# Optimization experiments

Hardware: AMD Instinct MI355X
Metric: run time of the kernel (lower is better)

## Reference

```python
import jax, jax.numpy as jnp
import numpy as np

B, P, ENC = 64, 196, 2048
H, A, E, V, T = 512, 512, 512, 10000, 20


def setup_inputs() -> dict:
    key = jax.random.key(0)
    ks = jax.random.split(key, 24)
    s = 0.02
    inp = {
        "encoder_out": jax.random.normal(ks[0], (B, P, ENC), jnp.float32),
        "captions": jax.random.randint(ks[1], (B, T), 0, V),
        "lengths": jnp.sort(jax.random.randint(ks[2], (B,), 5, T + 1))[::-1].at[0].set(T).astype(jnp.int32),
        # Attention
        "enc_att_w": jax.random.normal(ks[3], (A, ENC)) * s,
        "enc_att_b": jnp.zeros((A,)),
        "hid_att_w": jax.random.normal(ks[4], (A, H)) * s,
        "hid_att_b": jnp.zeros((A,)),
        "full_att_w": jax.random.normal(ks[5], (1, A)) * s,
        "full_att_b": jnp.zeros((1,)),
        # Embedding
        "embed_w": jax.random.uniform(ks[6], (V, E), minval=-0.1, maxval=0.1),
        # LSTMCell (input = embed + encoder -> E + ENC)
        "lstm_w_ih": jax.random.normal(ks[7], (4 * H, E + ENC)) * s,
        "lstm_w_hh": jax.random.normal(ks[8], (4 * H, H)) * s,
        "lstm_b_ih": jnp.zeros((4 * H,)),
        "lstm_b_hh": jnp.zeros((4 * H,)),
        # init hidden/cell from mean encoder features
        "init_h_w": jax.random.normal(ks[9], (H, ENC)) * s,
        "init_h_b": jnp.zeros((H,)),
        "init_c_w": jax.random.normal(ks[10], (H, ENC)) * s,
        "init_c_b": jnp.zeros((H,)),
        # gating
        "fbeta_w": jax.random.normal(ks[11], (ENC, H)) * s,
        "fbeta_b": jnp.zeros((ENC,)),
        # output fc
        "fc_w": jax.random.uniform(ks[12], (V, H), minval=-0.1, maxval=0.1),
        "fc_b": jnp.zeros((V,)),
    }
    return inp


def reference(encoder_out, captions, lengths,
              enc_att_w, enc_att_b, hid_att_w, hid_att_b, full_att_w, full_att_b,
              embed_w, lstm_w_ih, lstm_w_hh, lstm_b_ih, lstm_b_hh,
              init_h_w, init_h_b, init_c_w, init_c_b,
              fbeta_w, fbeta_b, fc_w, fc_b):
    emb = embed_w[captions]                      # [B, T, E]
    mean_enc = encoder_out.mean(axis=1)          # [B, ENC]
    h0 = mean_enc @ init_h_w.T + init_h_b
    c0 = mean_enc @ init_c_w.T + init_c_b
    # encoder attention projection is constant across timesteps
    att1 = encoder_out @ enc_att_w.T + enc_att_b  # [B, P, A]
    dec_len = lengths - 1                         # decode lengths per sample

    def step(carry, xs):
        h, c = carry
        emb_t, t = xs
        att2 = h @ hid_att_w.T + hid_att_b                     # [B, A]
        e = jax.nn.relu(att1 + att2[:, None, :]) @ full_att_w[0] + full_att_b[0]  # [B, P]
        alpha = jax.nn.softmax(e, axis=1)                       # [B, P]
        awe = jnp.einsum('bpe,bp->be', encoder_out, alpha)      # [B, ENC]
        gate = jax.nn.sigmoid(h @ fbeta_w.T + fbeta_b)
        x = jnp.concatenate([emb_t, gate * awe], axis=1)        # [B, E+ENC]
        gates = x @ lstm_w_ih.T + lstm_b_ih + h @ lstm_w_hh.T + lstm_b_hh
        i, f, g, o = jnp.split(gates, 4, axis=1)
        c_new = jax.nn.sigmoid(f) * c + jax.nn.sigmoid(i) * jnp.tanh(g)
        h_new = jax.nn.sigmoid(o) * jnp.tanh(c_new)
        pred = h_new @ fc_w.T + fc_b                            # [B, V]
        active = (t < dec_len)[:, None]
        h = jnp.where(active, h_new, h)
        c = jnp.where(active, c_new, c)
        pred = jnp.where(active, pred, jnp.zeros_like(pred))
        alpha = jnp.where(active, alpha, jnp.zeros_like(alpha))
        return (h, c), (pred, alpha)

    Tm1 = emb.shape[1] - 1
    ts = jnp.arange(Tm1)
    emb_seq = jnp.transpose(emb[:, :Tm1], (1, 0, 2))            # [T-1, B, E]
    (_, _), (preds, alphas) = jax.lax.scan(step, (h0, c0), (emb_seq, ts))
    predictions = jnp.transpose(preds, (1, 0, 2))               # [B, T-1, V]
    alphas = jnp.transpose(alphas, (1, 0, 2))                   # [B, T-1, P]
    return predictions, alphas
```

## Files before the change

kernel.cpp:

```cpp
#include <hip/hip_runtime.h>
#include <hip/hip_bf16.h>

typedef short short8  __attribute__((ext_vector_type(8)));
typedef float floatx4 __attribute__((ext_vector_type(4)));
typedef int   int4v   __attribute__((ext_vector_type(4)));

constexpr int BB = 64, PP = 196, CENC = 2048, HH = 512, AA = 512, EE = 512;
constexpr int VV = 10000, TT = 20, TM1 = 19;
constexpr int NCAT = 4608;

__device__ __forceinline__ float bf2f(short u) {
    union { unsigned u; float f; } v; v.u = ((unsigned)(unsigned short)u) << 16; return v.f;
}
__device__ __forceinline__ short f2bf(float f) {
    union { float f; unsigned u; } v; v.f = f;
    unsigned r = v.u + 0x7FFF + ((v.u >> 16) & 1);
    return (short)(r >> 16);
}

#define GLL(gp, lp) __builtin_amdgcn_global_load_lds( \
    (const __attribute__((address_space(1))) void*)(gp), \
    (__attribute__((address_space(3))) void*)(lp), 16, 0, 0)

__global__ __launch_bounds__(256)
void kPrepW(const float* __restrict__ encw_s, const float* __restrict__ haw,
            const float* __restrict__ fbw, const float* __restrict__ whh,
            const float* __restrict__ wih, const float* __restrict__ fcw,
            const float* __restrict__ ihw, const float* __restrict__ icw,
            const float* __restrict__ hab, const float* __restrict__ fbb,
            const float* __restrict__ bih, const float* __restrict__ bhh,
            const float* __restrict__ ihb, const float* __restrict__ icb,
            short* __restrict__ encw_d, short* __restrict__ wcat_d,
            short* __restrict__ wihe_d, short* __restrict__ wihm_d,
            short* __restrict__ fc_d, short* __restrict__ initW_d,
            float* __restrict__ biascat, float* __restrict__ biasg,
            float* __restrict__ biasInit)
{
    long e = ((long)blockIdx.x * 256 + threadIdx.x) * 8;
    const float* sp = nullptr; short* dp = nullptr; long de = 0;
    if (e < 1048576)       { sp = &encw_s[e]; dp = encw_d; de = e; }
    else if (e < 3407872)  { long u = e - 1048576; long row = u >> 9, col = u & 511;
                             sp = (row < 512) ? &haw[row * 512 + col]
                                : (row < 2560) ? &fbw[(row - 512) * 512 + col]
                                               : &whh[(row - 2560) * 512 + col];
                             dp = wcat_d; de = u; }
    else if (e < 7602176)  { long u = e - 3407872; long row = u >> 11, col = u & 2047;
                             sp = &wih[row * 2560 + 512 + col]; dp = wihe_d; de = u; }
    else if (e < 8650752)  { long u = e - 7602176; long row = u >> 9, col = u & 511;
                             sp = &wih[row * 2560 + col]; dp = wihm_d; de = u; }
    else if (e < 13770752) { long u = e - 8650752; sp = &fcw[u]; dp = fc_d; de = u; }
    else if (e < 15867904) { long u = e - 13770752;
                             sp = (u < 1048576) ? &ihw[u] : &icw[u - 1048576];
                             dp = initW_d; de = u; }
    else if (e < 15872512) { long u = e - 15867904;
                             for (int j = 0; j < 8; ++j) { long w = u + j;
                                 biascat[w] = (w < 512) ? hab[w] : ((w < 2560) ? fbb[w - 512] : 0.f); }
                             return; }
    else if (e < 15874560) { long u = e - 15872512;
                             for (int j = 0; j < 8; ++j) biasg[u + j] = bih[u + j] + bhh[u + j];
                             return; }
    else if (e < 15875584) { long u = e - 15874560;
                             for (int j = 0; j < 8; ++j) { long w = u + j;
                                 biasInit[w] = (w < 512) ? ihb[w] : icb[w - 512]; }
                             return; }
    else return;
    union { short s[8]; int4v v; } u8;
    #pragma unroll
    for (int j = 0; j < 8; ++j) u8.s[j] = f2bf(sp[j]);
    *reinterpret_cast<int4v*>(&dp[de]) = u8.v;
}

template<int FULL>
__global__ __launch_bounds__(256)
void kMeanEnc(const float* __restrict__ enc, short* __restrict__ enc16,
              float* __restrict__ meanP)
{
    int b = blockIdx.x, kc = blockIdx.y, pz = blockIdx.z;
    int k = kc * 256 + threadIdx.x;
    const float* eb = &enc[((size_t)b * PP + pz * 28) * CENC + k];
    short* ob = &enc16[((size_t)b * PP + pz * 28) * CENC + k];
    float s0 = 0, s1 = 0, s2 = 0, s3 = 0;
    for (int p = 0; p < 28; p += 4) {
        float v0 = eb[(size_t)(p + 0) * CENC], v1 = eb[(size_t)(p + 1) * CENC];
        float v2 = eb[(size_t)(p + 2) * CENC], v3 = eb[(size_t)(p + 3) * CENC];
        s0 += v0; s1 += v1; s2 += v2; s3 += v3;
        if (FULL) {
            ob[(size_t)(p + 0) * CENC] = f2bf(v0); ob[(size_t)(p + 1) * CENC] = f2bf(v1);
            ob[(size_t)(p + 2) * CENC] = f2bf(v2); ob[(size_t)(p + 3) * CENC] = f2bf(v3);
        }
    }
    meanP[((size_t)pz * 64 + b) * 2048 + k] = (s0 + s1) + (s2 + s3);
}

__global__ __launch_bounds__(256)
void kReduceMean(const float* __restrict__ meanP, short* __restrict__ mean16)
{
    int b = blockIdx.x, c0 = threadIdx.x * 8;
    const float inv = 1.0f / PP;
    union { short s[8]; int4v v; } u8;
    #pragma unroll
    for (int j = 0; j < 8; ++j) {
        float s = 0.f;
        #pragma unroll
        for (int pz = 0; pz < 7; ++pz) s += meanP[((size_t)pz * 64 + b) * 2048 + c0 + j];
        u8.s[j] = f2bf(s * inv);
    }
    *reinterpret_cast<int4v*>(&mean16[b * 2048 + c0]) = u8.v;
}

__global__ __launch_bounds__(256)
void kEmbGather(const float* __restrict__ embw, const int* __restrict__ captions,
                short* __restrict__ embA)
{
    long e = ((long)blockIdx.x * 256 + threadIdx.x) * 8;
    int r = (int)(e >> 9), j = (int)(e & 511);
    int t = r >> 6, b = r & 63;
    int tok = captions[b * TT + t];
    const float* sp = &embw[(size_t)tok * EE + j];
    union { short s[8]; int4v v; } u8;
    #pragma unroll
    for (int q = 0; q < 8; ++q) u8.s[q] = f2bf(sp[q]);
    *reinterpret_cast<int4v*>(&embA[e]) = u8.v;
}

template<int AOP, int WOP, int EOP, int SWZ>
__global__ __launch_bounds__(256)
void kGemm(const void* __restrict__ Ap, int lda, const short* __restrict__ W, int ldw,
           const float* __restrict__ bias, int Ntot,
           float* __restrict__ outF, int ldc, short* __restrict__ outB,
           int nk, const int* __restrict__ lengths)
{
    __shared__ short As[64 * 64];
    __shared__ short Ws[64 * 64];
    int nb, mb, kz;
    if (SWZ == 0) { nb = blockIdx.x; mb = blockIdx.y; kz = blockIdx.z; }
    else if (SWZ == 1) {
        int j = blockIdx.x;
        if (j < 1536) { mb = (j >> 6) * 8 + (j & 7); nb = (j >> 3) & 7; }
        else          { int u = j - 1536; mb = 192 + (u >> 3); nb = u & 7; }
        kz = 0;
    } else {
        int j = blockIdx.x; int c = j & 7, s = j >> 3;
        mb = s % 19; int u = s / 19; nb = 8 * u + c; kz = 0;
        if (nb * 64 >= Ntot) return;
    }
    const int tid = threadIdx.x;
    const int m0 = mb * 64, n0 = nb * 64, k0 = kz * nk * 64;
    const int w = tid >> 6, l = tid & 63;
    floatx4 acc[4] = {};

    for (int ks = 0; ks < nk; ++ks) {
        int kt = k0 + ks * 64;
        if (AOP == 0) {
            const short* A = (const short*)Ap;
            #pragma unroll
            for (int i = 0; i < 2; ++i) {
                int ii = w * 2 + i;
                int row = ii * 8 + (l >> 3);
                int cg = l & 7;
                const short* gp = &A[(size_t)(m0 + row) * lda + kt + ((cg ^ (row & 7)) << 3)];
                GLL(gp, &As[ii * 512]);
            }
        } else {
            const float* A = (const float*)Ap;
            #pragma unroll
            for (int i = 0; i < 2; ++i) {
                int s = tid + i * 256, row = s >> 3, cg = s & 7;
                const float* sp = &A[(size_t)(m0 + row) * lda + kt + cg * 8];
                float4 a = *reinterpret_cast<const float4*>(sp);
                float4 b = *reinterpret_cast<const float4*>(sp + 4);
                union { short s[8]; int4v v; } u8;
                u8.s[0]=f2bf(a.x); u8.s[1]=f2bf(a.y); u8.s[2]=f2bf(a.z); u8.s[3]=f2bf(a.w);
                u8.s[4]=f2bf(b.x); u8.s[5]=f2bf(b.y); u8.s[6]=f2bf(b.z); u8.s[7]=f2bf(b.w);
                *reinterpret_cast<int4v*>(&As[row * 64 + ((cg ^ (row & 7)) << 3)]) = u8.v;
            }
        }
        #pragma unroll
        for (int i = 0; i < 2; ++i) {
            int ii = w * 2 + i;
            int r = ii * 8 + (l >> 3);
            int cg = l & 7;
            int wr;
            if (WOP == 1) wr = 512 * (r >> 4) + 16 * nb + (r & 15);
            else          wr = n0 + r;
            if (WOP == 1 || wr < Ntot) {
                const short* gp = &W[(size_t)wr * ldw + kt + ((cg ^ (r & 7)) << 3)];
                GLL(gp, &Ws[ii * 512]);
            }
        }
        __syncthreads();
        #pragma unroll
        for (int kc = 0; kc < 2; ++kc) {
            int arow = 16 * w + (l & 15);
            int cg = 4 * kc + (l >> 4);
            short8 af = *reinterpret_cast<const short8*>(&As[arow * 64 + ((cg ^ (arow & 7)) << 3)]);
            #pragma unroll
            for (int q = 0; q < 4; ++q) {
                int wrow = 16 * q + (l & 15);
                short8 wf = *reinterpret_cast<const short8*>(&Ws[wrow * 64 + ((cg ^ (wrow & 7)) << 3)]);
                acc[q] = __builtin_amdgcn_mfma_f32_16x16x32_bf16(af, wf, acc[q], 0, 0, 0);
            }
        }
        __syncthreads();
    }
    int l4 = l >> 4, l15 = l & 15;
    #pragma unroll
    for (int q = 0; q < 4; ++q) {
        #pragma unroll
        for (int j = 0; j < 4; ++j) {
            int m = m0 + 16 * w + 4 * l4 + j;
            int n = n0 + 16 * q + l15;
            float val = acc[q][j];
            if (EOP == 0) {
                outF[(size_t)m * ldc + n] = val + bias[n];
            } else if (EOP == 1) {
                outB[(size_t)m * ldc + n] = f2bf(val + bias[n]);
            } else if (EOP == 2) {
                if (n < Ntot) {
                    int b = m & 63, tt = m >> 6;
                    bool act = tt < (lengths[b] - 1);
                    outF[((size_t)b * TM1 + tt) * VV + n] = act ? (val + bias[n]) : 0.f;
                }
            } else if (EOP == 3) {
                int mloc = m - m0;
                outF[((size_t)kz * 64 + mloc) * ldc + n] = val;
            } else {
                int col = 512 * q + (n0 >> 2) + l15;
                int mloc = m - m0;
                outF[((size_t)kz * 64 + mloc) * 2048 + col] = val;
            }
        }
    }
}

__global__ __launch_bounds__(256)
void kReduceHC(const float* __restrict__ Pc, const float* __restrict__ biasInit,
               float* __restrict__ hc, short* __restrict__ h16)
{
    int b = blockIdx.x, tid = threadIdx.x;
    for (int j = tid; j < 1024; j += 256) {
        float s = Pc[((size_t)0 * BB + b) * 1024 + j] + Pc[((size_t)1 * BB + b) * 1024 + j]
                + Pc[((size_t)2 * BB + b) * 1024 + j] + Pc[((size_t)3 * BB + b) * 1024 + j];
        s += biasInit[j];
        hc[b * 1024 + j] = s;
        if (j < 512) h16[b * 512 + j] = f2bf(s);
    }
}

template<int FULL>
__global__ __launch_bounds__(256)
void kStepBC(const short* __restrict__ att1, const float* __restrict__ P3h,
             const float* __restrict__ faw, const float* __restrict__ fab,
             const int* __restrict__ lengths, const void* __restrict__ encp,
             short* __restrict__ x16, float* __restrict__ alpha_out, int t)
{
    int blk = blockIdx.x, tid = threadIdx.x;
    int b = blk & 63, kc = blk >> 6;
    __shared__ float att2s[512];
    __shared__ float fw[512];
    __shared__ float es[PP];
    __shared__ float alps[PP];
    __shared__ float red[8];
    __shared__ float part[8][256];

    for (int a = tid; a < 512; a += 256) { att2s[a] = P3h[b * NCAT + a]; fw[a] = faw[a]; }
    __syncthreads();

    int wv = tid >> 6, lane = tid & 63;
    for (int p = wv; p < PP; p += 4) {
        short8 v = *reinterpret_cast<const short8*>(&att1[((size_t)b * PP + p) * 512 + lane * 8]);
        float s = 0.f;
        #pragma unroll
        for (int j = 0; j < 8; ++j) {
            float x = bf2f(v[j]) + att2s[lane * 8 + j];
            s += fmaxf(x, 0.f) * fw[lane * 8 + j];
        }
        #pragma unroll
        for (int off = 32; off > 0; off >>= 1) s += __shfl_down(s, off, 64);
        if (lane == 0) es[p] = s + fab[0];
    }
    __syncthreads();
    float m = -1e30f;
    for (int p = tid; p < PP; p += 256) m = fmaxf(m, es[p]);
    #pragma unroll
    for (int off = 32; off > 0; off >>= 1) m = fmaxf(m, __shfl_down(m, off, 64));
    if (lane == 0) red[wv] = m;
    __syncthreads();
    m = fmaxf(fmaxf(red[0], red[1]), fmaxf(red[2], red[3]));
    float ssum = 0.f;
    for (int p = tid; p < PP; p += 256) { float ev = __expf(es[p] - m); es[p] = ev; ssum += ev; }
    #pragma unroll
    for (int off = 32; off > 0; off >>= 1) ssum += __shfl_down(ssum, off, 64);
    if (lane == 0) red[4 + wv] = ssum;
    __syncthreads();
    float inv = 1.f / (red[4] + red[5] + red[6] + red[7]);
    bool active = t < (lengths[b] - 1);
    for (int p = tid; p < PP; p += 256) {
        float al = es[p] * inv;
        alps[p] = al;
        if (kc == 0)
            alpha_out[((size_t)b * TM1 + t) * PP + p] = active ? al : 0.f;
    }
    __syncthreads();

    if (FULL) {
        const short* enc16 = (const short*)encp;
        int g = tid & 31, prow = tid >> 5;
        int k0 = kc * 256 + g * 8;
        float acc[8] = {};
        for (int p = prow; p < PP; p += 8) {
            short8 v = *reinterpret_cast<const short8*>(&enc16[((size_t)b * PP + p) * CENC + k0]);
            float a_ = alps[p];
            #pragma unroll
            for (int j = 0; j < 8; ++j) acc[j] = fmaf(bf2f(v[j]), a_, acc[j]);
        }
        *reinterpret_cast<float4*>(&part[prow][g * 8])     = make_float4(acc[0], acc[1], acc[2], acc[3]);
        *reinterpret_cast<float4*>(&part[prow][g * 8 + 4]) = make_float4(acc[4], acc[5], acc[6], acc[7]);
        __syncthreads();
        int c = tid;
        float awe = 0.f;
        #pragma unroll
        for (int pr = 0; pr < 8; ++pr) awe += part[pr][c];
        int k = kc * 256 + c;
        float gate = 1.f / (1.f + __expf(-P3h[b * NCAT + 512 + k]));
        x16[(size_t)b * CENC + k] = f2bf(gate * awe);
    } else {
        const float* enc = (const float*)encp;
        int g = tid & 63, prow = tid >> 6;
        int k0 = kc * 256 + g * 4;
        float acc[4] = {};
        for (int p = prow; p < PP; p += 4) {
            float4 v = *reinterpret_cast<const float4*>(&enc[((size_t)b * PP + p) * CENC + k0]);
            float a_ = alps[p];
            acc[0] = fmaf(v.x, a_, acc[0]); acc[1] = fmaf(v.y, a_, acc[1]);
            acc[2] = fmaf(v.z, a_, acc[2]); acc[3] = fmaf(v.w, a_, acc[3]);
        }
        *reinterpret_cast<float4*>(&part[prow][g * 4]) = make_float4(acc[0], acc[1], acc[2], acc[3]);
        __syncthreads();
        int c = tid;
        float awe = part[0][c] + part[1][c] + part[2][c] + part[3][c];
        int k = kc * 256 + c;
        float gate = 1.f / (1.f + __expf(-P3h[b * NCAT + 512 + k]));
        x16[(size_t)b * CENC + k] = f2bf(gate * awe);
    }
}

__global__ __launch_bounds__(256)
void kStepD2(const float* __restrict__ Pg, const float* __restrict__ gates_emb,
             const float* __restrict__ P3h, float* __restrict__ hc,
             short* __restrict__ h16, short* __restrict__ allH, int t)
{
    int b = blockIdx.x, tid = threadIdx.x;
    for (int d = tid; d < 512; d += 256) {
        float g4[4];
        #pragma unroll
        for (int q = 0; q < 4; ++q) {
            int col = q * 512 + d;
            float s = gates_emb[((size_t)t * 64 + b) * 2048 + col] + P3h[b * NCAT + 2560 + col];
            #pragma unroll
            for (int kz = 0; kz < 4; ++kz) s += Pg[((size_t)kz * 64 + b) * 2048 + col];
            g4[q] = s;
        }
        float i_ = 1.f / (1.f + __expf(-g4[0]));
        float f_ = 1.f / (1.f + __expf(-g4[1]));
        float g_ = tanhf(g4[2]);
        float o_ = 1.f / (1.f + __expf(-g4[3]));
        float c_new = f_ * hc[b * 1024 + 512 + d] + i_ * g_;
        float h_new = o_ * tanhf(c_new);
        hc[b * 1024 + 512 + d] = c_new;
        hc[b * 1024 + d] = h_new;
        short hb = f2bf(h_new);
        h16[b * 512 + d] = hb;
        allH[((size_t)t * 64 + b) * 512 + d] = hb;
    }
}

extern "C" void kernel_launch(void* const* d_in, const int* in_sizes, int n_in,
                              void* d_out, int out_size, void* d_ws, size_t ws_size,
                              hipStream_t stream)
{
    const float* enc        = (const float*)d_in[0];
    const int*   captions   = (const int*)d_in[1];
    const int*   lengths    = (const int*)d_in[2];
    const float* enc_att_w  = (const float*)d_in[3];
    const float* enc_att_b  = (const float*)d_in[4];
    const float* hid_att_w  = (const float*)d_in[5];
    const float* hid_att_b  = (const float*)d_in[6];
    const float* full_att_w = (const float*)d_in[7];
    const float* full_att_b = (const float*)d_in[8];
    const float* embw       = (const float*)d_in[9];
    const float* w_ih       = (const float*)d_in[10];
    const float* w_hh       = (const float*)d_in[11];
    const float* b_ih       = (const float*)d_in[12];
    const float* b_hh       = (const float*)d_in[13];
    const float* init_h_w   = (const float*)d_in[14];
    const float* init_h_b   = (const float*)d_in[15];
    const float* init_c_w   = (const float*)d_in[16];
    const float* init_c_b   = (const float*)d_in[17];
    const float* fbeta_w    = (const float*)d_in[18];
    const float* fbeta_b    = (const float*)d_in[19];
    const float* fc_w       = (const float*)d_in[20];
    const float* fc_b       = (const float*)d_in[21];

    float* out_pred  = (float*)d_out;
    float* out_alpha = out_pred + (size_t)BB * TM1 * VV;

    char* pr = (char*)d_out;
    short* att1_16   = (short*)pr;  pr += 12845056;
    float* gates_emb = (float*)pr;  pr += 9961472;
    short* wcat16    = (short*)pr;  pr += 4718592;
    short* wihe16    = (short*)pr;  pr += 8388608;
    float* biascat   = (float*)pr;  pr += 18432;
    float* P3h       = (float*)pr;  pr += 1179648;
    float* Pg        = (float*)pr;  pr += 2097152;
    short* embA      = (short*)pr;  pr += 1245184;
    short* wihm16    = (short*)pr;  pr += 2097152;
    short* encw16    = (short*)pr;  pr += 2097152;
    float* biasg     = (float*)pr;  pr += 8192;
    float* meanP     = (float*)pr;  pr += 3670016;
    short* mean16    = (short*)pr;  pr += 262144;

    short* initW16  = (short*)gates_emb;
    float* biasInit = (float*)((char*)gates_emb + 4194304);
    float* hcP      = P3h;

    char* wp = (char*)d_ws;
    float* hc    = (float*)wp;  wp += 262144;
    short* h16   = (short*)wp;  wp += 65536;
    short* x16   = (short*)wp;  wp += 262144;
    short* fc16  = (short*)wp;  wp += 10240000;
    short* allH  = (short*)wp;  wp += 1245184;
    short* enc16 = (short*)wp;  wp += 51380224;
    const bool full = ((size_t)(wp - (char*)d_ws) <= ws_size);

    kPrepW<<<7752, 256, 0, stream>>>(enc_att_w, hid_att_w, fbeta_w, w_hh, w_ih, fc_w,
                                     init_h_w, init_c_w,
                                     hid_att_b, fbeta_b, b_ih, b_hh, init_h_b, init_c_b,
                                     encw16, wcat16, wihe16, wihm16, fc16, initW16,
                                     biascat, biasg, biasInit);
    if (full) kMeanEnc<1><<<dim3(64, 8, 7), 256, 0, stream>>>(enc, enc16, meanP);
    else      kMeanEnc<0><<<dim3(64, 8, 7), 256, 0, stream>>>(enc, enc16, meanP);
    kEmbGather<<<304, 256, 0, stream>>>(embw, captions, embA);
    kReduceMean<<<64, 256, 0, stream>>>(meanP, mean16);

    kGemm<0, 0, 3, 0><<<dim3(16, 1, 4), 256, 0, stream>>>(mean16, CENC, initW16, CENC,
        nullptr, 1024, hcP, 1024, nullptr, 8, nullptr);
    kReduceHC<<<64, 256, 0, stream>>>(hcP, biasInit, hc, h16);

    if (full)
        kGemm<0, 0, 1, 1><<<1568, 256, 0, stream>>>(enc16, CENC, encw16, CENC,
            enc_att_b, 512, nullptr, 512, att1_16, 32, nullptr);
    else
        kGemm<1, 0, 1, 1><<<1568, 256, 0, stream>>>(enc, CENC, encw16, CENC,
            enc_att_b, 512, nullptr, 512, att1_16, 32, nullptr);

    kGemm<0, 0, 0, 0><<<dim3(32, 19, 1), 256, 0, stream>>>(embA, 512, wihm16, 512,
        biasg, 2048, gates_emb, 2048, nullptr, 8, nullptr);

    for (int t = 0; t < TM1; ++t) {
        kGemm<0, 0, 0, 0><<<dim3(72, 1, 1), 256, 0, stream>>>(h16, 512, wcat16, 512,
            biascat, NCAT, P3h, NCAT, nullptr, 8, nullptr);

        if (full) kStepBC<1><<<512, 256, 0, stream>>>(att1_16, P3h, full_att_w,
            full_att_b, lengths, enc16, x16, out_alpha, t);
        else      kStepBC<0><<<512, 256, 0, stream>>>(att1_16, P3h, full_att_w,
            full_att_b, lengths, enc, x16, out_alpha, t);

        kGemm<0, 1, 4, 0><<<dim3(32, 1, 4), 256, 0, stream>>>(x16, CENC, wihe16, CENC,
            nullptr, 2048, Pg, 2048, nullptr, 8, nullptr);

        kStepD2<<<64, 256, 0, stream>>>(Pg, gates_emb, P3h, hc, h16, allH, t);
    }

    kGemm<0, 0, 2, 2><<<3040, 256, 0, stream>>>(allH, 512, fc16, 512,
        fc_b, VV, out_pred, VV, nullptr, 8, lengths);
}
```

Measured before the change: 1.228 ms.

## Restructure decoder step kernels and switch big GEMMs to 128x128 tiles

```diff
diff --git a/kernel.cpp b/kernel.cpp
--- a/kernel.cpp
+++ b/kernel.cpp
@@ -7,7 +7,6 @@
 
 constexpr int BB = 64, PP = 196, CENC = 2048, HH = 512, AA = 512, EE = 512;
 constexpr int VV = 10000, TT = 20, TM1 = 19;
-constexpr int NCAT = 4608;
 
 __device__ __forceinline__ float bf2f(short u) {
     union { unsigned u; float f; } v; v.u = ((unsigned)(unsigned short)u) << 16; return v.f;
@@ -27,44 +26,48 @@
             const float* __restrict__ fbw, const float* __restrict__ whh,
             const float* __restrict__ wih, const float* __restrict__ fcw,
             const float* __restrict__ ihw, const float* __restrict__ icw,
-            const float* __restrict__ hab, const float* __restrict__ fbb,
-            const float* __restrict__ bih, const float* __restrict__ bhh,
-            const float* __restrict__ ihb, const float* __restrict__ icb,
+            const float* __restrict__ fbb, const float* __restrict__ bih,
+            const float* __restrict__ bhh, const float* __restrict__ ihb,
+            const float* __restrict__ icb,
             short* __restrict__ encw_d, short* __restrict__ wcat_d,
             short* __restrict__ wihe_d, short* __restrict__ wihm_d,
             short* __restrict__ fc_d, short* __restrict__ initW_d,
-            float* __restrict__ biascat, float* __restrict__ biasg,
-            float* __restrict__ biasInit)
+            short* __restrict__ hidattT, float* __restrict__ biascat,
+            float* __restrict__ biasg, float* __restrict__ biasInit)
 {
     long e = ((long)blockIdx.x * 256 + threadIdx.x) * 8;
+    union { short s[8]; int4v v; } u8;
     const float* sp = nullptr; short* dp = nullptr; long de = 0;
     if (e < 1048576)       { sp = &encw_s[e]; dp = encw_d; de = e; }
-    else if (e < 3407872)  { long u = e - 1048576; long row = u >> 9, col = u & 511;
-                             sp = (row < 512) ? &haw[row * 512 + col]
-                                : (row < 2560) ? &fbw[(row - 512) * 512 + col]
-                                               : &whh[(row - 2560) * 512 + col];
+    else if (e < 3145728)  { long u = e - 1048576; long row = u >> 9, col = u & 511;
+                             sp = (row < 2048) ? &fbw[row * 512 + col]
+                                               : &whh[(row - 2048) * 512 + col];
                              dp = wcat_d; de = u; }
-    else if (e < 7602176)  { long u = e - 3407872; long row = u >> 11, col = u & 2047;
+    else if (e < 7340032)  { long u = e - 3145728; long row = u >> 11, col = u & 2047;
                              sp = &wih[row * 2560 + 512 + col]; dp = wihe_d; de = u; }
-    else if (e < 8650752)  { long u = e - 7602176; long row = u >> 9, col = u & 511;
+    else if (e < 8388608)  { long u = e - 7340032; long row = u >> 9, col = u & 511;
                              sp = &wih[row * 2560 + col]; dp = wihm_d; de = u; }
-    else if (e < 13770752) { long u = e - 8650752; sp = &fcw[u]; dp = fc_d; de = u; }
-    else if (e < 15867904) { long u = e - 13770752;
+    else if (e < 13508608) { long u = e - 8388608; sp = &fcw[u]; dp = fc_d; de = u; }
+    else if (e < 15605760) { long u = e - 13508608;
                              sp = (u < 1048576) ? &ihw[u] : &icw[u - 1048576];
                              dp = initW_d; de = u; }
-    else if (e < 15872512) { long u = e - 15867904;
+    else if (e < 15867904) { long u = e - 15605760; long k = u >> 9, a0 = u & 511;
+                             #pragma unroll
+                             for (int j = 0; j < 8; ++j) u8.s[j] = f2bf(haw[(a0 + j) * 512 + k]);
+                             *reinterpret_cast<int4v*>(&hidattT[u]) = u8.v;
+                             return; }
+    else if (e < 15872000) { long u = e - 15867904;
                              for (int j = 0; j < 8; ++j) { long w = u + j;
-                                 biascat[w] = (w < 512) ? hab[w] : ((w < 2560) ? fbb[w - 512] : 0.f); }
+                                 biascat[w] = (w < 2048) ? fbb[w] : 0.f; }
                              return; }
-    else if (e < 15874560) { long u = e - 15872512;
+    else if (e < 15874048) { long u = e - 15872000;
                              for (int j = 0; j < 8; ++j) biasg[u + j] = bih[u + j] + bhh[u + j];
                              return; }
-    else if (e < 15875584) { long u = e - 15874560;
+    else if (e < 15875072) { long u = e - 15874048;
                              for (int j = 0; j < 8; ++j) { long w = u + j;
                                  biasInit[w] = (w < 512) ? ihb[w] : icb[w - 512]; }
                              return; }
     else return;
-    union { short s[8]; int4v v; } u8;
     #pragma unroll
     for (int j = 0; j < 8; ++j) u8.s[j] = f2bf(sp[j]);
     *reinterpret_cast<int4v*>(&dp[de]) = u8.v;
@@ -123,27 +126,15 @@
     *reinterpret_cast<int4v*>(&embA[e]) = u8.v;
 }
 
-template<int AOP, int WOP, int EOP, int SWZ>
-__global__ __launch_bounds__(256)
-void kGemm(const void* __restrict__ Ap, int lda, const short* __restrict__ W, int ldw,
-           const float* __restrict__ bias, int Ntot,
-           float* __restrict__ outF, int ldc, short* __restrict__ outB,
-           int nk, const int* __restrict__ lengths)
+template<int EOP>
+__global__ __launch_bounds__(256)
+void kGemm(const short* __restrict__ A, int lda, const short* __restrict__ W, int ldw,
+           const float* __restrict__ bias,
+           float* __restrict__ outF, int ldc, int nk)
 {
     __shared__ short As[64 * 64];
     __shared__ short Ws[64 * 64];
-    int nb, mb, kz;
-    if (SWZ == 0) { nb = blockIdx.x; mb = blockIdx.y; kz = blockIdx.z; }
-    else if (SWZ == 1) {
-        int j = blockIdx.x;
-        if (j < 1536) { mb = (j >> 6) * 8 + (j & 7); nb = (j >> 3) & 7; }
-        else          { int u = j - 1536; mb = 192 + (u >> 3); nb = u & 7; }
-        kz = 0;
-    } else {
-        int j = blockIdx.x; int c = j & 7, s = j >> 3;
-        mb = s % 19; int u = s / 19; nb = 8 * u + c; kz = 0;
-        if (nb * 64 >= Ntot) return;
-    }
+    const int nb = blockIdx.x, mb = blockIdx.y, kz = blockIdx.z;
     const int tid = threadIdx.x;
     const int m0 = mb * 64, n0 = nb * 64, k0 = kz * nk * 64;
     const int w = tid >> 6, l = tid & 63;
@@ -151,20 +142,91 @@
 
     for (int ks = 0; ks < nk; ++ks) {
         int kt = k0 + ks * 64;
+        #pragma unroll
+        for (int i = 0; i < 2; ++i) {
+            int ii = w * 2 + i;
+            int row = ii * 8 + (l >> 3), cg = l & 7;
+            GLL(&A[(size_t)(m0 + row) * lda + kt + ((cg ^ (row & 7)) << 3)], &As[ii * 512]);
+        }
+        #pragma unroll
+        for (int i = 0; i < 2; ++i) {
+            int ii = w * 2 + i;
+            int r = ii * 8 + (l >> 3), cg = l & 7;
+            GLL(&W[(size_t)(n0 + r) * ldw + kt + ((cg ^ (r & 7)) << 3)], &Ws[ii * 512]);
+        }
+        __syncthreads();
+        #pragma unroll
+        for (int kc = 0; kc < 2; ++kc) {
+            int arow = 16 * w + (l & 15);
+            int cg = 4 * kc + (l >> 4);
+            short8 af = *reinterpret_cast<const short8*>(&As[arow * 64 + ((cg ^ (arow & 7)) << 3)]);
+            #pragma unroll
+            for (int q = 0; q < 4; ++q) {
+                int wrow = 16 * q + (l & 15);
+                short8 wf = *reinterpret_cast<const short8*>(&Ws[wrow * 64 + ((cg ^ (wrow & 7)) << 3)]);
+                acc[q] = __builtin_amdgcn_mfma_f32_16x16x32_bf16(af, wf, acc[q], 0, 0, 0);
+            }
+        }
+        __syncthreads();
+    }
+    int l4 = l >> 4, l15 = l & 15;
+    #pragma unroll
+    for (int q = 0; q < 4; ++q) {
+        #pragma unroll
+        for (int j = 0; j < 4; ++j) {
+            int m = m0 + 16 * w + 4 * l4 + j;
+            int n = n0 + 16 * q + l15;
+            float val = acc[q][j];
+            if (EOP == 0) {
+                outF[(size_t)m * ldc + n] = val + bias[n];
+            } else {
+                int mloc = m - m0;
+                outF[((size_t)kz * 64 + mloc) * ldc + n] = val;
+            }
+        }
+    }
+}
+
+template<int AOP, int EOP, int SWZ>
+__global__ __launch_bounds__(256)
+void kGemm128(const void* __restrict__ Ap, int lda, const short* __restrict__ W, int ldw,
+              const float* __restrict__ bias, int Ntot, int Mtot,
+              float* __restrict__ outF, short* __restrict__ outB, int ldc,
+              int nk, const int* __restrict__ lengths)
+{
+    __shared__ short As[128 * 64];
+    __shared__ short Ws[128 * 64];
+    int mb, nb;
+    if (SWZ == 1) {
+        int o = blockIdx.x;
+        int wg = (o & 7) * 49 + (o >> 3);
+        mb = wg >> 2; nb = wg & 3;
+    } else {
+        int o = blockIdx.x;
+        int x = o & 7, idx = o >> 3;
+        int base = (x < 6) ? x * 99 : 594 + (x - 6) * 98;
+        int wg = base + idx;
+        mb = wg % 10; nb = wg / 10;
+    }
+    const int tid = threadIdx.x, w = tid >> 6, l = tid & 63;
+    const int m0 = mb * 128, n0 = nb * 128;
+    const int l4 = l >> 4, l15 = l & 15;
+    floatx4 acc[2][8] = {};
+
+    for (int ks = 0; ks < nk; ++ks) {
+        int kt = ks * 64;
         if (AOP == 0) {
             const short* A = (const short*)Ap;
             #pragma unroll
-            for (int i = 0; i < 2; ++i) {
-                int ii = w * 2 + i;
-                int row = ii * 8 + (l >> 3);
-                int cg = l & 7;
-                const short* gp = &A[(size_t)(m0 + row) * lda + kt + ((cg ^ (row & 7)) << 3)];
-                GLL(gp, &As[ii * 512]);
+            for (int i = 0; i < 4; ++i) {
+                int ii = w * 4 + i;
+                int row = ii * 8 + (l >> 3), cg = l & 7;
+                GLL(&A[(size_t)(m0 + row) * lda + kt + ((cg ^ (row & 7)) << 3)], &As[ii * 512]);
             }
         } else {
             const float* A = (const float*)Ap;
             #pragma unroll
-            for (int i = 0; i < 2; ++i) {
+            for (int i = 0; i < 4; ++i) {
                 int s = tid + i * 256, row = s >> 3, cg = s & 7;
                 const float* sp = &A[(size_t)(m0 + row) * lda + kt + cg * 8];
                 float4 a = *reinterpret_cast<const float4*>(sp);
@@ -176,58 +238,50 @@
             }
         }
         #pragma unroll
-        for (int i = 0; i < 2; ++i) {
-            int ii = w * 2 + i;
-            int r = ii * 8 + (l >> 3);
-            int cg = l & 7;
-            int wr;
-            if (WOP == 1) wr = 512 * (r >> 4) + 16 * nb + (r & 15);
-            else          wr = n0 + r;
-            if (WOP == 1 || wr < Ntot) {
-                const short* gp = &W[(size_t)wr * ldw + kt + ((cg ^ (r & 7)) << 3)];
-                GLL(gp, &Ws[ii * 512]);
-            }
+        for (int i = 0; i < 4; ++i) {
+            int ii = w * 4 + i;
+            int r = ii * 8 + (l >> 3), cg = l & 7;
+            GLL(&W[(size_t)(n0 + r) * ldw + kt + ((cg ^ (r & 7)) << 3)], &Ws[ii * 512]);
         }
         __syncthreads();
         #pragma unroll
         for (int kc = 0; kc < 2; ++kc) {
-            int arow = 16 * w + (l & 15);
-            int cg = 4 * kc + (l >> 4);
-            short8 af = *reinterpret_cast<const short8*>(&As[arow * 64 + ((cg ^ (arow & 7)) << 3)]);
-            #pragma unroll
-            for (int q = 0; q < 4; ++q) {
-                int wrow = 16 * q + (l & 15);
+            int cg = 4 * kc + l4;
+            short8 af0, af1;
+            {
+                int ar0 = 32 * w + l15;
+                int ar1 = 32 * w + 16 + l15;
+                af0 = *reinterpret_cast<const short8*>(&As[ar0 * 64 + ((cg ^ (ar0 & 7)) << 3)]);
+                af1 = *reinterpret_cast<const short8*>(&As[ar1 * 64 + ((cg ^ (ar1 & 7)) << 3)]);
+            }
+            #pragma unroll
+            for (int q = 0; q < 8; ++q) {
+                int wrow = 16 * q + l15;
                 short8 wf = *reinterpret_cast<const short8*>(&Ws[wrow * 64 + ((cg ^ (wrow & 7)) << 3)]);
-                acc[q] = __builtin_amdgcn_mfma_f32_16x16x32_bf16(af, wf, acc[q], 0, 0, 0);
-            }
-        }
-        __syncthreads();
-    }
-    int l4 = l >> 4, l15 = l & 15;
+                acc[0][q] = __builtin_amdgcn_mfma_f32_16x16x32_bf16(af0, wf, acc[0][q], 0, 0, 0);
+                acc[1][q] = __builtin_amdgcn_mfma_f32_16x16x32_bf16(af1, wf, acc[1][q], 0, 0, 0);
+            }
+        }
+        __syncthreads();
+    }
     #pragma unroll
-    for (int q = 0; q < 4; ++q) {
-        #pragma unroll
-        for (int j = 0; j < 4; ++j) {
-            int m = m0 + 16 * w + 4 * l4 + j;
-            int n = n0 + 16 * q + l15;
-            float val = acc[q][j];
-            if (EOP == 0) {
-                outF[(size_t)m * ldc + n] = val + bias[n];
-            } else if (EOP == 1) {
-                outB[(size_t)m * ldc + n] = f2bf(val + bias[n]);
-            } else if (EOP == 2) {
-                if (n < Ntot) {
-                    int b = m & 63, tt = m >> 6;
-                    bool act = tt < (lengths[b] - 1);
-                    outF[((size_t)b * TM1 + tt) * VV + n] = act ? (val + bias[n]) : 0.f;
+    for (int sm = 0; sm < 2; ++sm) {
+        #pragma unroll
+        for (int q = 0; q < 8; ++q) {
+            #pragma unroll
+            for (int j = 0; j < 4; ++j) {
+                int m = m0 + 32 * w + 16 * sm + 4 * l4 + j;
+                int n = n0 + 16 * q + l15;
+                float val = acc[sm][q][j];
+                if (EOP == 1) {
+                    outB[(size_t)m * ldc + n] = f2bf(val + bias[n]);
+                } else {
+                    if (m < Mtot && n < Ntot) {
+                        int b = m & 63, tt = m >> 6;
+                        bool act = tt < (lengths[b] - 1);
+                        outF[((size_t)b * TM1 + tt) * VV + n] = act ? (val + bias[n]) : 0.f;
+                    }
                 }
-            } else if (EOP == 3) {
-                int mloc = m - m0;
-                outF[((size_t)kz * 64 + mloc) * ldc + n] = val;
-            } else {
-                int col = 512 * q + (n0 >> 2) + l15;
-                int mloc = m - m0;
-                outF[((size_t)kz * 64 + mloc) * 2048 + col] = val;
             }
         }
     }
@@ -247,60 +301,135 @@
     }
 }
 
+__global__ __launch_bounds__(256)
+void kStepA(const short* __restrict__ h16, const short* __restrict__ wcat16,
+            const float* __restrict__ biascat, const short* __restrict__ hidattT,
+            const float* __restrict__ hid_att_b, const short* __restrict__ att1,
+            const float* __restrict__ faw, const float* __restrict__ fab,
+            const int* __restrict__ lengths, float* __restrict__ P3h,
+            float* __restrict__ alphaG, float* __restrict__ out_alpha, int t)
+{
+    __shared__ __align__(16) char smem[16384];
+    const int blk = blockIdx.x, tid = threadIdx.x;
+    const int w = tid >> 6, l = tid & 63;
+
+    if (blk < 64) {
+        short* As = (short*)smem;
+        short* Ws = (short*)(smem + 8192);
+        const int n0 = blk * 64;
+        floatx4 acc[4] = {};
+        for (int ks = 0; ks < 8; ++ks) {
+            int kt = ks * 64;
+            #pragma unroll
+            for (int i = 0; i < 2; ++i) {
+                int ii = w * 2 + i;
+                int row = ii * 8 + (l >> 3), cg = l & 7;
+                GLL(&h16[row * 512 + kt + ((cg ^ (row & 7)) << 3)], &As[ii * 512]);
+            }
+            #pragma unroll
+            for (int i = 0; i < 2; ++i) {
+                int ii = w * 2 + i;
+                int r = ii * 8 + (l >> 3), cg = l & 7;
+                GLL(&wcat16[(size_t)(n0 + r) * 512 + kt + ((cg ^ (r & 7)) << 3)], &Ws[ii * 512]);
+            }
+            __syncthreads();
+            #pragma unroll
+            for (int kc = 0; kc < 2; ++kc) {
+                int arow = 16 * w + (l & 15);
+                int cg = 4 * kc + (l >> 4);
+                short8 af = *reinterpret_cast<const short8*>(&As[arow * 64 + ((cg ^ (arow & 7)) << 3)]);
+                #pragma unroll
+                for (int q = 0; q < 4; ++q) {
+                    int wrow = 16 * q + (l & 15);
+                    short8 wf = *reinterpret_cast<const short8*>(&Ws[wrow * 64 + ((cg ^ (wrow & 7)) << 3)]);
+                    acc[q] = __builtin_amdgcn_mfma_f32_16x16x32_bf16(af, wf, acc[q], 0, 0, 0);
+                }
+            }
+            __syncthreads();
+        }
+        int l4 = l >> 4, l15 = l & 15;
+        #pragma unroll
+        for (int q = 0; q < 4; ++q)
+            #pragma unroll
+            for (int j = 0; j < 4; ++j) {
+                int m = 16 * w + 4 * l4 + j;
+                int n = n0 + 16 * q + l15;
+                P3h[m * 4096 + n] = acc[q][j] + biascat[n];
+            }
+    } else {
+        const int b = blk - 64;
+        float* hsh   = (float*)smem;
+        float* att2s = (float*)(smem + 2048);
+        float* fwsh  = (float*)(smem + 4096);
+        float* es    = (float*)(smem + 6144);
+        float* red   = (float*)(smem + 7040);
+
+        hsh[tid]       = bf2f(h16[b * 512 + tid]);
+        hsh[tid + 256] = bf2f(h16[b * 512 + tid + 256]);
+        fwsh[tid]       = faw[tid];
+        fwsh[tid + 256] = faw[tid + 256];
+        __syncthreads();
+
+        {
+            float s0 = hid_att_b[tid], s1 = hid_att_b[tid + 256];
+            for (int k = 0; k < 512; k += 8) {
+                #pragma unroll
+                for (int j = 0; j < 8; ++j) {
+                    float hk = hsh[k + j];
+                    s0 = fmaf(bf2f(hidattT[(k + j) * 512 + tid]), hk, s0);
+                    s1 = fmaf(bf2f(hidattT[(k + j) * 512 + tid + 256]), hk, s1);
+                }
+            }
+            att2s[tid] = s0; att2s[tid + 256] = s1;
+        }
+        __syncthreads();
+
+        for (int p = w; p < PP; p += 4) {
+            short8 v = *reinterpret_cast<const short8*>(&att1[((size_t)b * PP + p) * 512 + l * 8]);
+            float s = 0.f;
+            #pragma unroll
+            for (int j = 0; j < 8; ++j) {
+                float x = bf2f(v[j]) + att2s[l * 8 + j];
+                s += fmaxf(x, 0.f) * fwsh[l * 8 + j];
+            }
+            #pragma unroll
+            for (int off = 32; off > 0; off >>= 1) s += __shfl_down(s, off, 64);
+            if (l == 0) es[p] = s + fab[0];
+        }
+        __syncthreads();
+        float m = -1e30f;
+        for (int p = tid; p < PP; p += 256) m = fmaxf(m, es[p]);
+        #pragma unroll
+        for (int off = 32; off > 0; off >>= 1) m = fmaxf(m, __shfl_down(m, off, 64));
+        if (l == 0) red[w] = m;
+        __syncthreads();
+        m = fmaxf(fmaxf(red[0], red[1]), fmaxf(red[2], red[3]));
+        float ssum = 0.f;
+        for (int p = tid; p < PP; p += 256) { float ev = __expf(es[p] - m); es[p] = ev; ssum += ev; }
+        #pragma unroll
+        for (int off = 32; off > 0; off >>= 1) ssum += __shfl_down(ssum, off, 64);
+        if (l == 0) red[4 + w] = ssum;
+        __syncthreads();
+        float inv = 1.f / (red[4] + red[5] + red[6] + red[7]);
+        bool active = t < (lengths[b] - 1);
+        for (int p = tid; p < PP; p += 256) {
+            float al = es[p] * inv;
+            alphaG[b * PP + p] = al;
+            out_alpha[((size_t)b * TM1 + t) * PP + p] = active ? al : 0.f;
+        }
+    }
+}
+
 template<int FULL>
 __global__ __launch_bounds__(256)
-void kStepBC(const short* __restrict__ att1, const float* __restrict__ P3h,
-             const float* __restrict__ faw, const float* __restrict__ fab,
-             const int* __restrict__ lengths, const void* __restrict__ encp,
-             short* __restrict__ x16, float* __restrict__ alpha_out, int t)
+void kStepC(const float* __restrict__ alphaG, const float* __restrict__ P3h,
+            const void* __restrict__ encp, short* __restrict__ x16)
 {
     int blk = blockIdx.x, tid = threadIdx.x;
     int b = blk & 63, kc = blk >> 6;
-    __shared__ float att2s[512];
-    __shared__ float fw[512];
-    __shared__ float es[PP];
     __shared__ float alps[PP];
-    __shared__ float red[8];
     __shared__ float part[8][256];
-
-    for (int a = tid; a < 512; a += 256) { att2s[a] = P3h[b * NCAT + a]; fw[a] = faw[a]; }
-    __syncthreads();
-
-    int wv = tid >> 6, lane = tid & 63;
-    for (int p = wv; p < PP; p += 4) {
-        short8 v = *reinterpret_cast<const short8*>(&att1[((size_t)b * PP + p) * 512 + lane * 8]);
-        float s = 0.f;
-        #pragma unroll
-        for (int j = 0; j < 8; ++j) {
-            float x = bf2f(v[j]) + att2s[lane * 8 + j];
-            s += fmaxf(x, 0.f) * fw[lane * 8 + j];
-        }
-        #pragma unroll
-        for (int off = 32; off > 0; off >>= 1) s += __shfl_down(s, off, 64);
-        if (lane == 0) es[p] = s + fab[0];
-    }
-    __syncthreads();
-    float m = -1e30f;
-    for (int p = tid; p < PP; p += 256) m = fmaxf(m, es[p]);
-    #pragma unroll
-    for (int off = 32; off > 0; off >>= 1) m = fmaxf(m, __shfl_down(m, off, 64));
-    if (lane == 0) red[wv] = m;
-    __syncthreads();
-    m = fmaxf(fmaxf(red[0], red[1]), fmaxf(red[2], red[3]));
-    float ssum = 0.f;
-    for (int p = tid; p < PP; p += 256) { float ev = __expf(es[p] - m); es[p] = ev; ssum += ev; }
-    #pragma unroll
-    for (int off = 32; off > 0; off >>= 1) ssum += __shfl_down(ssum, off, 64);
-    if (lane == 0) red[4 + wv] = ssum;
-    __syncthreads();
-    float inv = 1.f / (red[4] + red[5] + red[6] + red[7]);
-    bool active = t < (lengths[b] - 1);
-    for (int p = tid; p < PP; p += 256) {
-        float al = es[p] * inv;
-        alps[p] = al;
-        if (kc == 0)
-            alpha_out[((size_t)b * TM1 + t) * PP + p] = active ? al : 0.f;
-    }
+    for (int p = tid; p < PP; p += 256) alps[p] = alphaG[b * PP + p];
     __syncthreads();
 
     if (FULL) {
@@ -322,7 +451,7 @@
         #pragma unroll
         for (int pr = 0; pr < 8; ++pr) awe += part[pr][c];
         int k = kc * 256 + c;
-        float gate = 1.f / (1.f + __expf(-P3h[b * NCAT + 512 + k]));
+        float gate = 1.f / (1.f + __expf(-P3h[b * 4096 + k]));
         x16[(size_t)b * CENC + k] = f2bf(gate * awe);
     } else {
         const float* enc = (const float*)encp;
@@ -340,38 +469,73 @@
         int c = tid;
         float awe = part[0][c] + part[1][c] + part[2][c] + part[3][c];
         int k = kc * 256 + c;
-        float gate = 1.f / (1.f + __expf(-P3h[b * NCAT + 512 + k]));
+        float gate = 1.f / (1.f + __expf(-P3h[b * 4096 + k]));
         x16[(size_t)b * CENC + k] = f2bf(gate * awe);
     }
 }
 
 __global__ __launch_bounds__(256)
-void kStepD2(const float* __restrict__ Pg, const float* __restrict__ gates_emb,
-             const float* __restrict__ P3h, float* __restrict__ hc,
-             short* __restrict__ h16, short* __restrict__ allH, int t)
-{
-    int b = blockIdx.x, tid = threadIdx.x;
-    for (int d = tid; d < 512; d += 256) {
-        float g4[4];
-        #pragma unroll
-        for (int q = 0; q < 4; ++q) {
-            int col = q * 512 + d;
-            float s = gates_emb[((size_t)t * 64 + b) * 2048 + col] + P3h[b * NCAT + 2560 + col];
-            #pragma unroll
-            for (int kz = 0; kz < 4; ++kz) s += Pg[((size_t)kz * 64 + b) * 2048 + col];
-            g4[q] = s;
-        }
-        float i_ = 1.f / (1.f + __expf(-g4[0]));
-        float f_ = 1.f / (1.f + __expf(-g4[1]));
-        float g_ = tanhf(g4[2]);
-        float o_ = 1.f / (1.f + __expf(-g4[3]));
-        float c_new = f_ * hc[b * 1024 + 512 + d] + i_ * g_;
+void kStepD(const short* __restrict__ x16, const short* __restrict__ wihe16,
+            const float* __restrict__ P3h, const float* __restrict__ gates_emb,
+            float* __restrict__ hc, short* __restrict__ h16,
+            short* __restrict__ allH, int t)
+{
+    __shared__ short As[64 * 64];
+    __shared__ short Ws[64 * 64];
+    const int nb = blockIdx.x, tid = threadIdx.x;
+    const int w = tid >> 6, l = tid & 63;
+    const int l4 = l >> 4, l15 = l & 15;
+    floatx4 acc[4] = {};
+
+    for (int ks = 0; ks < 32; ++ks) {
+        int kt = ks * 64;
+        #pragma unroll
+        for (int i = 0; i < 2; ++i) {
+            int ii = w * 2 + i;
+            int row = ii * 8 + (l >> 3), cg = l & 7;
+            GLL(&x16[row * 2048 + kt + ((cg ^ (row & 7)) << 3)], &As[ii * 512]);
+        }
+        #pragma unroll
+        for (int i = 0; i < 2; ++i) {
+            int ii = w * 2 + i;
+            int r = ii * 8 + (l >> 3), cg = l & 7;
+            int wr = 512 * (r >> 4) + 16 * nb + (r & 15);
+            GLL(&wihe16[(size_t)wr * 2048 + kt + ((cg ^ (r & 7)) << 3)], &Ws[ii * 512]);
+        }
+        __syncthreads();
+        #pragma unroll
+        for (int kc = 0; kc < 2; ++kc) {
+            int arow = 16 * w + l15;
+            int cg = 4 * kc + l4;
+            short8 af = *reinterpret_cast<const short8*>(&As[arow * 64 + ((cg ^ (arow & 7)) << 3)]);
+            #pragma unroll
+            for (int q = 0; q < 4; ++q) {
+                int wrow = 16 * q + l15;
+                short8 wf = *reinterpret_cast<const short8*>(&Ws[wrow * 64 + ((cg ^ (wrow & 7)) << 3)]);
+                acc[q] = __builtin_amdgcn_mfma_f32_16x16x32_bf16(af, wf, acc[q], 0, 0, 0);
+            }
+        }
+        __syncthreads();
+    }
+
+    const int d = 16 * nb + l15;
+    #pragma unroll
+    for (int j = 0; j < 4; ++j) {
+        int m = 16 * w + 4 * l4 + j;
+        float g0 = acc[0][j] + gates_emb[((size_t)t * 64 + m) * 2048 +    0 + d] + P3h[m * 4096 + 2048 +    0 + d];
+        float g1 = acc[1][j] + gates_emb[((size_t)t * 64 + m) * 2048 +  512 + d] + P3h[m * 4096 + 2048 +  512 + d];
+        float g2 = acc[2][j] + gates_emb[((size_t)t * 64 + m) * 2048 + 1024 + d] + P3h[m * 4096 + 2048 + 1024 + d];
+        float g3 = acc[3][j] + gates_emb[((size_t)t * 64 + m) * 2048 + 1536 + d] + P3h[m * 4096 + 2048 + 1536 + d];
+        float i_ = 1.f / (1.f + __expf(-g0));
+        float f_ = 1.f / (1.f + __expf(-g1));
+        float gg = tanhf(g2);
+        float o_ = 1.f / (1.f + __expf(-g3));
+        float c_new = f_ * hc[m * 1024 + 512 + d] + i_ * gg;
         float h_new = o_ * tanhf(c_new);
-        hc[b * 1024 + 512 + d] = c_new;
-        hc[b * 1024 + d] = h_new;
+        hc[m * 1024 + 512 + d] = c_new;
         short hb = f2bf(h_new);
-        h16[b * 512 + d] = hb;
-        allH[((size_t)t * 64 + b) * 512 + d] = hb;
+        h16[m * 512 + d] = hb;
+        allH[((size_t)t * 64 + m) * 512 + d] = hb;
     }
 }
 
@@ -408,15 +572,16 @@
     char* pr = (char*)d_out;
     short* att1_16   = (short*)pr;  pr += 12845056;
     float* gates_emb = (float*)pr;  pr += 9961472;
-    short* wcat16    = (short*)pr;  pr += 4718592;
+    short* wcat16    = (short*)pr;  pr += 4194304;
     short* wihe16    = (short*)pr;  pr += 8388608;
-    float* biascat   = (float*)pr;  pr += 18432;
-    float* P3h       = (float*)pr;  pr += 1179648;
-    float* Pg        = (float*)pr;  pr += 2097152;
+    float* biascat   = (float*)pr;  pr += 16384;
+    float* P3h       = (float*)pr;  pr += 1048576;
+    float* alphaG    = (float*)pr;  pr += 50176;
+    short* hidattT   = (short*)pr;  pr += 524288;
+    float* biasg     = (float*)pr;  pr += 8192;
     short* embA      = (short*)pr;  pr += 1245184;
     short* wihm16    = (short*)pr;  pr += 2097152;
     short* encw16    = (short*)pr;  pr += 2097152;
-    float* biasg     = (float*)pr;  pr += 8192;
     float* meanP     = (float*)pr;  pr += 3670016;
     short* mean16    = (short*)pr;  pr += 262144;
 
@@ -428,50 +593,46 @@
     float* hc    = (float*)wp;  wp += 262144;
     short* h16   = (short*)wp;  wp += 65536;
     short* x16   = (short*)wp;  wp += 262144;
+    short* allH  = (short*)wp;  wp += 1245184;
     short* fc16  = (short*)wp;  wp += 10240000;
-    short* allH  = (short*)wp;  wp += 1245184;
+    wp += 131072;
     short* enc16 = (short*)wp;  wp += 51380224;
     const bool full = ((size_t)(wp - (char*)d_ws) <= ws_size);
 
     kPrepW<<<7752, 256, 0, stream>>>(enc_att_w, hid_att_w, fbeta_w, w_hh, w_ih, fc_w,
                                      init_h_w, init_c_w,
-                                     hid_att_b, fbeta_b, b_ih, b_hh, init_h_b, init_c_b,
+                                     fbeta_b, b_ih, b_hh, init_h_b, init_c_b,
                                      encw16, wcat16, wihe16, wihm16, fc16, initW16,
-                                     biascat, biasg, biasInit);
+                                     hidattT, biascat, biasg, biasInit);
     if (full) kMeanEnc<1><<<dim3(64, 8, 7), 256, 0, stream>>>(enc, enc16, meanP);
     else      kMeanEnc<0><<<dim3(64, 8, 7), 256, 0, stream>>>(enc, enc16, meanP);
     kEmbGather<<<304, 256, 0, stream>>>(embw, captions, embA);
     kReduceMean<<<64, 256, 0, stream>>>(meanP, mean16);
 
-    kGemm<0, 0, 3, 0><<<dim3(16, 1, 4), 256, 0, stream>>>(mean16, CENC, initW16, CENC,
-        nullptr, 1024, hcP, 1024, nullptr, 8, nullptr);
+    kGemm<3><<<dim3(16, 1, 4), 256, 0, stream>>>(mean16, CENC, initW16, CENC,
+        nullptr, hcP, 1024, 8);
     kReduceHC<<<64, 256, 0, stream>>>(hcP, biasInit, hc, h16);
 
     if (full)
-        kGemm<0, 0, 1, 1><<<1568, 256, 0, stream>>>(enc16, CENC, encw16, CENC,
-            enc_att_b, 512, nullptr, 512, att1_16, 32, nullptr);
+        kGemm128<0, 1, 1><<<392, 256, 0, stream>>>(enc16, CENC, encw16, CENC,
+            enc_att_b, 512, 12544, nullptr, att1_16, 512, 32, nullptr);
     else
-        kGemm<1, 0, 1, 1><<<1568, 256, 0, stream>>>(enc, CENC, encw16, CENC,
-            enc_att_b, 512, nullptr, 512, att1_16, 32, nullptr);
-
-    kGemm<0, 0, 0, 0><<<dim3(32, 19, 1), 256, 0, stream>>>(embA, 512, wihm16, 512,
-        biasg, 2048, gates_emb, 2048, nullptr, 8, nullptr);
+        kGemm128<1, 1, 1><<<392, 256, 0, stream>>>(enc, CENC, encw16, CENC,
+            enc_att_b, 512, 12544, nullptr, att1_16, 512, 32, nullptr);
+
+    kGemm<0><<<dim3(32, 19, 1), 256, 0, stream>>>(embA, 512, wihm16, 512,
+        biasg, gates_emb, 2048, 8);
 
     for (int t = 0; t < TM1; ++t) {
-        kGemm<0, 0, 0, 0><<<dim3(72, 1, 1), 256, 0, stream>>>(h16, 512, wcat16, 512,
-            biascat, NCAT, P3h, NCAT, nullptr, 8, nullptr);
-
-        if (full) kStepBC<1><<<512, 256, 0, stream>>>(att1_16, P3h, full_att_w,
-            full_att_b, lengths, enc16, x16, out_alpha, t);
-        else      kStepBC<0><<<512, 256, 0, stream>>>(att1_16, P3h, full_att_w,
-            full_att_b, lengths, enc, x16, out_alpha, t);
-
-        kGemm<0, 1, 4, 0><<<dim3(32, 1, 4), 256, 0, stream>>>(x16, CENC, wihe16, CENC,
-            nullptr, 2048, Pg, 2048, nullptr, 8, nullptr);
-
-        kStepD2<<<64, 256, 0, stream>>>(Pg, gates_emb, P3h, hc, h16, allH, t);
-    }
-
-    kGemm<0, 0, 2, 2><<<3040, 256, 0, stream>>>(allH, 512, fc16, 512,
-        fc_b, VV, out_pred, VV, nullptr, 8, lengths);
-}
+        kStepA<<<128, 256, 0, stream>>>(h16, wcat16, biascat, hidattT, hid_att_b,
+            att1_16, full_att_w, full_att_b, lengths, P3h, alphaG, out_alpha, t);
+
+        if (full) kStepC<1><<<512, 256, 0, stream>>>(alphaG, P3h, enc16, x16);
+        else      kStepC<0><<<512, 256, 0, stream>>>(alphaG, P3h, enc, x16);
+
+        kStepD<<<32, 256, 0, stream>>>(x16, wihe16, P3h, gates_emb, hc, h16, allH, t);
+    }
+
+    kGemm128<0, 2, 2><<<790, 256, 0, stream>>>(allH, 512, fc16, 512,
+        fc_b, VV, TM1 * BB, out_pred, nullptr, VV, 8, lengths);
+}
```

After: 1.853 ms. 50.9% more time.
